# Optimization experiments

Measured on AMD Instinct MI355X. Metric: run time of the kernel, lower is better.

Reference implementation:

```python
import jax, jax.numpy as jnp
import numpy as np

N_NODES = 50000
N_EDGES = 1_600_000
N_GRAPHS = 64
EMB = 1280
GCN_DIMS = [128, 256, 256]
FC_DIMS = [1024, 128]
EPS = 1e-5  # BatchNorm eps (torch default)


def setup_inputs() -> dict:
    key = jax.random.key(0)
    ks = jax.random.split(key, 16)
    inp = {}
    inp["x"] = jax.random.normal(ks[0], (N_NODES, EMB), jnp.float32)
    inp["edge_index"] = jax.random.randint(ks[1], (2, N_EDGES), 0, N_NODES)
    inp["batch"] = jnp.sort(jax.random.randint(ks[2], (N_NODES,), 0, N_GRAPHS))
    dims = [EMB] + GCN_DIMS
    for i in range(3):
        inp[f"Wg{i}"] = jax.random.normal(ks[3 + i], (dims[i], dims[i + 1]), jnp.float32) * (1.0 / np.sqrt(dims[i]))
        inp[f"bg{i}"] = jnp.zeros((dims[i + 1],), jnp.float32)
        inp[f"gamma{i}"] = jnp.ones((dims[i + 1],), jnp.float32)
        inp[f"beta{i}"] = jnp.zeros((dims[i + 1],), jnp.float32)
    fdims = [GCN_DIMS[-1]] + FC_DIMS
    for i in range(2):
        inp[f"Wf{i}"] = jax.random.normal(ks[10 + i], (fdims[i], fdims[i + 1]), jnp.float32) * (1.0 / np.sqrt(fdims[i]))
        inp[f"bf{i}"] = jnp.zeros((fdims[i + 1],), jnp.float32)
    return inp


def _batchnorm(h, gamma, beta):
    # training-mode BN over node dim, biased variance (torch normalization)
    m = h.mean(axis=0)
    v = h.var(axis=0)
    return gamma * (h - m) * jax.lax.rsqrt(v + EPS) + beta


def reference(x, edge_index, batch,
              Wg0, bg0, gamma0, beta0,
              Wg1, bg1, gamma1, beta1,
              Wg2, bg2, gamma2, beta2,
              Wf0, bf0, Wf1, bf1):
    # --- GCN symmetric normalization with self-loops (PyG GCNConv default) ---
    loop = jnp.arange(N_NODES)
    src = jnp.concatenate([edge_index[0], loop])  # message sources
    dst = jnp.concatenate([edge_index[1], loop])  # aggregation targets
    deg = jax.ops.segment_sum(jnp.ones(src.shape[0], jnp.float32), dst, num_segments=N_NODES)
    dinv = jnp.where(deg > 0, jax.lax.rsqrt(jnp.maximum(deg, 1.0)), 0.0)
    norm = dinv[src] * dinv[dst]  # [E + N]

    def gcn_conv(h, W, b):
        h = h @ W                               # [N, d_out] transform first (PyG order)
        msg = h[src] * norm[:, None]            # gather + scale
        return jax.ops.segment_sum(msg, dst, num_segments=N_NODES) + b

    h = x
    for W, b, g, bt in ((Wg0, bg0, gamma0, beta0),
                        (Wg1, bg1, gamma1, beta1),
                        (Wg2, bg2, gamma2, beta2)):
        h = gcn_conv(h, W, b)
        h = _batchnorm(h, g, bt)
        h = jax.nn.relu(h)
        # dropout is identity in eval mode

    # --- global mean pool over graphs ---
    counts = jax.ops.segment_sum(jnp.ones(N_NODES, jnp.float32), batch, num_segments=N_GRAPHS)
    sums = jax.ops.segment_sum(h, batch, num_segments=N_GRAPHS)
    g = sums / jnp.maximum(counts, 1.0)[:, None]  # [B, 256]

    # --- FC head ---
    g = jax.nn.relu(g @ Wf0 + bf0)
    out = g @ Wf1 + bf1                           # [B, 128]
    return out
```

## Files before the change

### kernel.cpp

```cpp
#include <hip/hip_runtime.h>
#include <hip/hip_bf16.h>

#define N_NODES 50000
#define N_EDGES 1600000
#define N_GRAPHS 64

typedef _Float16 f16;
typedef _Float16 f16x8 __attribute__((ext_vector_type(8)));
typedef _Float16 f16x4 __attribute__((ext_vector_type(4)));
typedef _Float16 f16x2 __attribute__((ext_vector_type(2)));
typedef float f32x4 __attribute__((ext_vector_type(4)));

template <int V> struct VecT;
template <> struct VecT<2> { using type = f16x2; };
template <> struct VecT<4> { using type = f16x4; };

typedef __attribute__((address_space(3))) void lds_void_t;
typedef const __attribute__((address_space(1))) void gbl_void_t;
__device__ __forceinline__ void gload_lds16(const void* g, void* l) {
    __builtin_amdgcn_global_load_lds((gbl_void_t*)g, (lds_void_t*)l, 16, 0, 0);
}

__global__ void init_deg(int* deg) {
    int i = blockIdx.x * blockDim.x + threadIdx.x;
    if (i < N_NODES) deg[i] = 1;
}

__global__ void deg_count(const int* __restrict__ dst, int* __restrict__ deg) {
    int e = blockIdx.x * blockDim.x + threadIdx.x;
    if (e < N_EDGES) atomicAdd(&deg[dst[e]], 1);
}

__global__ void make_dinv(const int* __restrict__ deg, float* __restrict__ dinv) {
    int i = blockIdx.x * blockDim.x + threadIdx.x;
    if (i < N_NODES) dinv[i] = rsqrtf((float)deg[i]);
}

__global__ void scan_deg(const int* __restrict__ deg, int* __restrict__ rowstart,
                         int* __restrict__ pos) {
    __shared__ int wsum[16];
    __shared__ int carry_s;
    const int t = threadIdx.x;
    const int lane = t & 63;
    const int w = t >> 6;
    if (t == 0) carry_s = 0;
    __syncthreads();
    for (int base = 0; base < N_NODES; base += 1024) {
        int i = base + t;
        int v = (i < N_NODES) ? (deg[i] - 1) : 0;
        int s = v;
#pragma unroll
        for (int off = 1; off < 64; off <<= 1) {
            int n = __shfl_up(s, off, 64);
            if (lane >= off) s += n;
        }
        if (lane == 63) wsum[w] = s;
        __syncthreads();
        if (w == 0) {
            int ws = (lane < 16) ? wsum[lane] : 0;
#pragma unroll
            for (int off = 1; off < 16; off <<= 1) {
                int n = __shfl_up(ws, off, 64);
                if (lane >= off) ws += n;
            }
            if (lane < 16) wsum[lane] = ws;
        }
        __syncthreads();
        int waveoff = (w == 0) ? 0 : wsum[w - 1];
        int carry = carry_s;
        int excl = carry + waveoff + s - v;
        if (i < N_NODES) {
            rowstart[i] = excl;
            pos[i] = excl;
        }
        __syncthreads();
        if (t == 0) carry_s = carry + wsum[15];
        __syncthreads();
    }
    if (t == 0) rowstart[N_NODES] = carry_s;
}

__global__ void csr_fill(const int* __restrict__ src, const int* __restrict__ dst,
                         const float* __restrict__ dinv, int* __restrict__ pos,
                         int2* __restrict__ csr) {
    int e = blockIdx.x * blockDim.x + threadIdx.x;
    if (e >= N_EDGES) return;
    int s = src[e], d = dst[e];
    int slot = atomicAdd(&pos[d], 1);
    csr[slot] = make_int2(s, __float_as_int(dinv[s] * dinv[d]));
}

__global__ void cast_w(const float* __restrict__ W, f16* __restrict__ Wt, int K, int N) {
    int i = blockIdx.x * blockDim.x + threadIdx.x;
    if (i >= K * N) return;
    int k = i % K, n = i / K;
    Wt[i] = (f16)W[(size_t)k * N + n];
}

__launch_bounds__(256)
__global__ void gemm_x_lds(const float* __restrict__ A, const f16* __restrict__ Bt,
                           float* __restrict__ C0, float* __restrict__ C1, int M) {
    const int K = 1280;
    __shared__ float Asm[128 * 32];
    const int t = threadIdx.x;
    const int w = t >> 6, lane = t & 63;
    const int tile = blockIdx.x >> 1, s = blockIdx.x & 1;
    const int m0 = tile * 128;
    const int kbeg = s * 640;
    float* __restrict__ C = s ? C1 : C0;
    const int r = lane & 15, q = lane >> 4;

    const int rl_base = w * 32 + (lane >> 3);
    const int gchunk = (lane & 7) ^ ((lane >> 3) & 7);

    const int row_l0 = w * 32 + r;
    const int row_l1 = w * 32 + 16 + r;
    const int sw = r & 7;
    const float* lr0a = Asm + row_l0 * 32 + (((2 * q) ^ sw) << 2);
    const float* lr0b = Asm + row_l0 * 32 + (((2 * q + 1) ^ sw) << 2);
    const float* lr1a = Asm + row_l1 * 32 + (((2 * q) ^ sw) << 2);
    const float* lr1b = Asm + row_l1 * 32 + (((2 * q + 1) ^ sw) << 2);

    const f16* bp = Bt + (size_t)r * K + kbeg + q * 8;

    f32x4 acc[2][8];
#pragma unroll
    for (int i = 0; i < 2; ++i)
#pragma unroll
        for (int j = 0; j < 8; ++j) acc[i][j] = (f32x4){0.f, 0.f, 0.f, 0.f};

    for (int kt = 0; kt < 20; ++kt) {
        const int kk = kbeg + kt * 32;
#pragma unroll
        for (int i = 0; i < 4; ++i) {
            int row_g = m0 + rl_base + i * 8;
            row_g = row_g < M ? row_g : M - 1;
            const float* src = A + (size_t)row_g * K + kk + gchunk * 4;
            float* dst = Asm + (w * 32 + i * 8) * 32;
            gload_lds16(src, dst);
        }
        __syncthreads();
        float4 u0 = *(const float4*)lr0a;
        float4 v0 = *(const float4*)lr0b;
        float4 u1 = *(const float4*)lr1a;
        float4 v1 = *(const float4*)lr1b;
        f16x8 af0 = {(f16)u0.x, (f16)u0.y, (f16)u0.z, (f16)u0.w,
                     (f16)v0.x, (f16)v0.y, (f16)v0.z, (f16)v0.w};
        f16x8 af1 = {(f16)u1.x, (f16)u1.y, (f16)u1.z, (f16)u1.w,
                     (f16)v1.x, (f16)v1.y, (f16)v1.z, (f16)v1.w};
#pragma unroll
        for (int ni = 0; ni < 8; ++ni) {
            f16x8 bf = *(const f16x8*)(bp + (size_t)ni * 16 * K + kt * 32);
            acc[0][ni] = __builtin_amdgcn_mfma_f32_16x16x32_f16(af0, bf, acc[0][ni], 0, 0, 0);
            acc[1][ni] = __builtin_amdgcn_mfma_f32_16x16x32_f16(af1, bf, acc[1][ni], 0, 0, 0);
        }
        __syncthreads();
    }
#pragma unroll
    for (int mi = 0; mi < 2; ++mi)
#pragma unroll
        for (int j = 0; j < 4; ++j) {
            int row = m0 + w * 32 + mi * 16 + q * 4 + j;
            if (row < M) {
                float* cp = C + (size_t)row * 128 + r;
#pragma unroll
                for (int ni = 0; ni < 8; ++ni) cp[ni * 16] = acc[mi][ni][j];
            }
        }
}

__global__ void reduce_cast(const float* __restrict__ c0, const float* __restrict__ c1,
                            f16* __restrict__ o, int n4) {
    int i = blockIdx.x * blockDim.x + threadIdx.x;
    if (i >= n4) return;
    float4 a = ((const float4*)c0)[i];
    float4 b = ((const float4*)c1)[i];
    f16x4 r = {(f16)(a.x + b.x), (f16)(a.y + b.y), (f16)(a.z + b.z), (f16)(a.w + b.w)};
    ((f16x4*)o)[i] = r;
}

template <int K>
__launch_bounds__(256)
__global__ void gemm_h_bn_pipe(const f16* __restrict__ A16, const float* __restrict__ ss,
                               const f16* __restrict__ Bt, f16* __restrict__ C16, int N) {
    constexpr int NT = K / 32;
    const int gw = (int)((blockIdx.x * blockDim.x + threadIdx.x) >> 6);
    const int lane = threadIdx.x & 63;
    const int m0 = gw * 32;
    if (m0 >= N_NODES) return;
    const int col0 = blockIdx.y * 128;
    const int r = lane & 15, q = lane >> 4;
    int row0 = m0 + r;       row0 = row0 < N_NODES ? row0 : N_NODES - 1;
    int row1 = m0 + 16 + r;  row1 = row1 < N_NODES ? row1 : N_NODES - 1;
    const f16* a0 = A16 + (size_t)row0 * K + q * 8;
    const f16* a1 = A16 + (size_t)row1 * K + q * 8;
    const f16* bp = Bt + (size_t)(col0 + r) * K + q * 8;
    const float* scp = ss + q * 8;
    const float* shp = ss + K + q * 8;

    f32x4 acc[2][8];
#pragma unroll
    for (int i = 0; i < 2; ++i)
#pragma unroll
        for (int j = 0; j < 8; ++j) acc[i][j] = (f32x4){0.f, 0.f, 0.f, 0.f};

    f16x8 ab[2][2];
    f16x8 bb[2][8];
    float4 sb[2][4];
    ab[0][0] = *(const f16x8*)(a0);
    ab[0][1] = *(const f16x8*)(a1);
    sb[0][0] = *(const float4*)(scp);
    sb[0][1] = *(const float4*)(scp + 4);
    sb[0][2] = *(const float4*)(shp);
    sb[0][3] = *(const float4*)(shp + 4);
#pragma unroll
    for (int ni = 0; ni < 8; ++ni) bb[0][ni] = *(const f16x8*)(bp + (size_t)ni * 16 * K);

#pragma unroll
    for (int kt = 0; kt < NT; ++kt) {
        const int cur = kt & 1, nxt = cur ^ 1;
        if (kt < NT - 1) {
            const int ko = (kt + 1) * 32;
            ab[nxt][0] = *(const f16x8*)(a0 + ko);
            ab[nxt][1] = *(const f16x8*)(a1 + ko);
            sb[nxt][0] = *(const float4*)(scp + ko);
            sb[nxt][1] = *(const float4*)(scp + ko + 4);
            sb[nxt][2] = *(const float4*)(shp + ko);
            sb[nxt][3] = *(const float4*)(shp + ko + 4);
#pragma unroll
            for (int ni = 0; ni < 8; ++ni)
                bb[nxt][ni] = *(const f16x8*)(bp + (size_t)ni * 16 * K + ko);
        }
        float sc[8] = {sb[cur][0].x, sb[cur][0].y, sb[cur][0].z, sb[cur][0].w,
                       sb[cur][1].x, sb[cur][1].y, sb[cur][1].z, sb[cur][1].w};
        float sh[8] = {sb[cur][2].x, sb[cur][2].y, sb[cur][2].z, sb[cur][2].w,
                       sb[cur][3].x, sb[cur][3].y, sb[cur][3].z, sb[cur][3].w};
        f16x8 af0, af1;
#pragma unroll
        for (int j = 0; j < 8; ++j) {
            float v0 = (float)ab[cur][0][j] * sc[j] + sh[j];
            float v1 = (float)ab[cur][1][j] * sc[j] + sh[j];
            af0[j] = (f16)(v0 > 0.f ? v0 : 0.f);
            af1[j] = (f16)(v1 > 0.f ? v1 : 0.f);
        }
#pragma unroll
        for (int ni = 0; ni < 8; ++ni) {
            acc[0][ni] = __builtin_amdgcn_mfma_f32_16x16x32_f16(af0, bb[cur][ni], acc[0][ni], 0, 0, 0);
            acc[1][ni] = __builtin_amdgcn_mfma_f32_16x16x32_f16(af1, bb[cur][ni], acc[1][ni], 0, 0, 0);
        }
    }
#pragma unroll
    for (int mi = 0; mi < 2; ++mi)
#pragma unroll
        for (int j = 0; j < 4; ++j) {
            int row = m0 + mi * 16 + q * 4 + j;
            if (row < N_NODES) {
                f16* cp = C16 + (size_t)row * N + col0 + r;
#pragma unroll
                for (int ni = 0; ni < 8; ++ni) cp[ni * 16] = (f16)acc[mi][ni][j];
            }
        }
}

template <int D>
__launch_bounds__(256)
__global__ void aggregate(const f16* __restrict__ h, const int* __restrict__ rowstart,
                          const int2* __restrict__ csr, const float* __restrict__ dinv,
                          const float* __restrict__ bias, f16* __restrict__ out) {
    constexpr int V = D / 64;
    using vec = typename VecT<V>::type;
    int w = (int)((blockIdx.x * blockDim.x + threadIdx.x) >> 6);
    int lane = threadIdx.x & 63;
    if (w >= N_NODES) return;
    float acc[V];
    float di = dinv[w];
    vec self = *(const vec*)(h + (size_t)w * D + lane * V);
#pragma unroll
    for (int v = 0; v < V; ++v) acc[v] = (float)self[v] * (di * di);
    int e0 = rowstart[w], e1 = rowstart[w + 1];
    int j = e0;
    for (; j + 8 <= e1; j += 8) {
        int2 c[8];
        vec rr[8];
#pragma unroll
        for (int u = 0; u < 8; ++u) c[u] = csr[j + u];
#pragma unroll
        for (int u = 0; u < 8; ++u)
            rr[u] = *(const vec*)(h + (size_t)c[u].x * D + lane * V);
#pragma unroll
        for (int u = 0; u < 8; ++u) {
            float nm = __int_as_float(c[u].y);
#pragma unroll
            for (int v = 0; v < V; ++v) acc[v] += (float)rr[u][v] * nm;
        }
    }
    if (j + 4 <= e1) {
        int2 c0 = csr[j], c1 = csr[j + 1], c2 = csr[j + 2], c3 = csr[j + 3];
        vec r0 = *(const vec*)(h + (size_t)c0.x * D + lane * V);
        vec r1 = *(const vec*)(h + (size_t)c1.x * D + lane * V);
        vec r2 = *(const vec*)(h + (size_t)c2.x * D + lane * V);
        vec r3 = *(const vec*)(h + (size_t)c3.x * D + lane * V);
        float n0 = __int_as_float(c0.y), n1 = __int_as_float(c1.y);
        float n2 = __int_as_float(c2.y), n3 = __int_as_float(c3.y);
#pragma unroll
        for (int v = 0; v < V; ++v)
            acc[v] += (float)r0[v] * n0 + (float)r1[v] * n1 +
                      (float)r2[v] * n2 + (float)r3[v] * n3;
        j += 4;
    }
    for (; j < e1; ++j) {
        int2 c = csr[j];
        vec r = *(const vec*)(h + (size_t)c.x * D + lane * V);
        float nm = __int_as_float(c.y);
#pragma unroll
        for (int v = 0; v < V; ++v) acc[v] += (float)r[v] * nm;
    }
    vec o;
#pragma unroll
    for (int v = 0; v < V; ++v) o[v] = (f16)(acc[v] + bias[lane * V + v]);
    *(vec*)(out + (size_t)w * D + lane * V) = o;
}

template <int D>
__global__ void bn_stats(const f16* __restrict__ h, float* __restrict__ stat) {
    int f = threadIdx.x;
    int r0 = blockIdx.x * 128;
    int r1 = min(r0 + 128, N_NODES);
    float s = 0.f, s2 = 0.f;
    for (int r = r0; r < r1; ++r) {
        float v = (float)h[(size_t)r * D + f];
        s += v;
        s2 += v * v;
    }
    atomicAdd(&stat[f], s);
    atomicAdd(&stat[D + f], s2);
}

template <int D>
__global__ void bn_finalize(const float* __restrict__ stat, const float* __restrict__ gamma,
                            const float* __restrict__ beta, float* __restrict__ ss) {
    int f = threadIdx.x;
    float m = stat[f] * (1.0f / N_NODES);
    float var = stat[D + f] * (1.0f / N_NODES) - m * m;
    float sc = gamma[f] * rsqrtf(var + 1e-5f);
    ss[f] = sc;
    ss[D + f] = beta[f] - m * sc;
}

__global__ void count_batch_bs(const int* __restrict__ batch, int* __restrict__ cnt) {
    int g = threadIdx.x;
    if (g >= N_GRAPHS) return;
    int lo = 0, hi = N_NODES;
    while (lo < hi) { int mid = (lo + hi) >> 1; if (batch[mid] < g) lo = mid + 1; else hi = mid; }
    int b0 = lo;
    lo = 0; hi = N_NODES;
    while (lo < hi) { int mid = (lo + hi) >> 1; if (batch[mid] < g + 1) lo = mid + 1; else hi = mid; }
    cnt[g] = lo - b0;
}

__global__ void pool_seg_bn(const f16* __restrict__ h, const float* __restrict__ ss,
                            const int* __restrict__ batch, float* __restrict__ psum) {
    int f = threadIdx.x;
    float sc = ss[f], sh = ss[256 + f];
    int r0 = blockIdx.x * 64;
    int r1 = min(r0 + 64, N_NODES);
    float acc = 0.f;
    int cur = batch[r0];
    for (int r = r0; r < r1; ++r) {
        int b = batch[r];
        if (b != cur) {
            atomicAdd(&psum[cur * 256 + f], acc);
            acc = 0.f;
            cur = b;
        }
        float v = sc * (float)h[(size_t)r * 256 + f] + sh;
        acc += v > 0.f ? v : 0.f;
    }
    atomicAdd(&psum[cur * 256 + f], acc);
}

__global__ void pool_div(const float* __restrict__ psum, const int* __restrict__ cnt,
                         float* __restrict__ g) {
    int i = blockIdx.x * 256 + threadIdx.x;
    int b = i >> 8;
    float c = (float)max(cnt[b], 1);
    g[i] = psum[i] / c;
}

__global__ void fc_init(const float* __restrict__ b, float* __restrict__ Y, int rows, int N) {
    int i = blockIdx.x * blockDim.x + threadIdx.x;
    if (i < rows * N) Y[i] = b[i % N];
}

__global__ void fc_splitk(const float* __restrict__ X, const float* __restrict__ W,
                          float* __restrict__ Y, int K, int N, int KC) {
    int col = blockIdx.x * blockDim.x + threadIdx.x;
    int row = blockIdx.y;
    int k0 = blockIdx.z * KC;
    float acc = 0.f;
    const float* x = X + (size_t)row * K + k0;
    const float* w = W + (size_t)k0 * N + col;
#pragma unroll 8
    for (int k = 0; k < KC; ++k) acc += x[k] * w[(size_t)k * N];
    atomicAdd(&Y[(size_t)row * N + col], acc);
}

__global__ void relu_inplace(float* __restrict__ Y, int n) {
    int i = blockIdx.x * blockDim.x + threadIdx.x;
    if (i < n) Y[i] = Y[i] > 0.f ? Y[i] : 0.f;
}

extern "C" void kernel_launch(void* const* d_in, const int* in_sizes, int n_in,
                              void* d_out, int out_size, void* d_ws, size_t ws_size,
                              hipStream_t stream) {
    const float* x     = (const float*)d_in[0];
    const int*   ei    = (const int*)d_in[1];
    const int*   batch = (const int*)d_in[2];
    const float* Wg0 = (const float*)d_in[3],  *bg0 = (const float*)d_in[4];
    const float* gamma0 = (const float*)d_in[5], *beta0 = (const float*)d_in[6];
    const float* Wg1 = (const float*)d_in[7],  *bg1 = (const float*)d_in[8];
    const float* gamma1 = (const float*)d_in[9], *beta1 = (const float*)d_in[10];
    const float* Wg2 = (const float*)d_in[11], *bg2 = (const float*)d_in[12];
    const float* gamma2 = (const float*)d_in[13], *beta2 = (const float*)d_in[14];
    const float* Wf0 = (const float*)d_in[15], *bf0 = (const float*)d_in[16];
    const float* Wf1 = (const float*)d_in[17], *bf1 = (const float*)d_in[18];
    float* out = (float*)d_out;

    size_t off = 0;
    auto alloc = [&](size_t bytes) {
        void* p = (char*)d_ws + off;
        off += (bytes + 255) & ~(size_t)255;
        return p;
    };
    f16*   hA16     = (f16*)alloc((size_t)N_NODES * 256 * 2);
    float* cp32     = (float*)alloc((size_t)2 * N_NODES * 128 * 4);
    f16*   hBn16    = (f16*)cp32;
    float* cp0      = cp32;
    float* cp1      = cp32 + (size_t)N_NODES * 128;
    int2*  csr      = (int2*)alloc((size_t)N_EDGES * 8);
    int*   deg      = (int*)alloc((size_t)N_NODES * 4);
    float* dinv     = (float*)alloc((size_t)N_NODES * 4);
    int*   rowstart = (int*)alloc((size_t)(N_NODES + 1) * 4);
    int*   pos      = (int*)alloc((size_t)N_NODES * 4);
    float* bnstat   = (float*)alloc(2 * 256 * 4);
    float* bnss     = (float*)alloc(2 * 256 * 4);
    float* psum     = (float*)alloc(64 * 256 * 4);
    int*   pcount   = (int*)alloc(64 * 4);
    float* gpool    = (float*)alloc(64 * 256 * 4);
    float* g1       = (float*)alloc(64 * 1024 * 4);
    f16*   W0t      = (f16*)alloc((size_t)1280 * 128 * 2);
    f16*   W1t      = (f16*)alloc((size_t)128 * 256 * 2);
    f16*   W2t      = (f16*)alloc((size_t)256 * 256 * 2);
    (void)ws_size;

    const int TPB = 256;
    const int nb_nodes = (N_NODES + TPB - 1) / TPB;
    const int nb_edges = (N_EDGES + TPB - 1) / TPB;

    init_deg<<<nb_nodes, TPB, 0, stream>>>(deg);
    deg_count<<<nb_edges, TPB, 0, stream>>>(ei + N_EDGES, deg);
    make_dinv<<<nb_nodes, TPB, 0, stream>>>(deg, dinv);
    scan_deg<<<1, 1024, 0, stream>>>(deg, rowstart, pos);
    csr_fill<<<nb_edges, TPB, 0, stream>>>(ei, ei + N_EDGES, dinv, pos, csr);
    cast_w<<<(1280 * 128 + 255) / 256, 256, 0, stream>>>(Wg0, W0t, 1280, 128);
    cast_w<<<(128 * 256 + 255) / 256, 256, 0, stream>>>(Wg1, W1t, 128, 256);
    cast_w<<<(256 * 256 + 255) / 256, 256, 0, stream>>>(Wg2, W2t, 256, 256);

    const int tiles128 = (N_NODES + 127) / 128;
    const int gemm0_blocks = tiles128 * 2;
    const int gemmh_blocks = (1563 * 64 + TPB - 1) / TPB;
    const int agg_blocks = (N_NODES * 64 + TPB - 1) / TPB;

    gemm_x_lds<<<gemm0_blocks, TPB, 0, stream>>>(x, W0t, cp0, cp1, N_NODES);
    reduce_cast<<<(N_NODES * 128 / 4 + 255) / 256, 256, 0, stream>>>(cp0, cp1, hA16, N_NODES * 128 / 4);
    aggregate<128><<<agg_blocks, TPB, 0, stream>>>(hA16, rowstart, csr, dinv, bg0, hBn16);
    hipMemsetAsync(bnstat, 0, 2 * 128 * 4, stream);
    bn_stats<128><<<(N_NODES + 127) / 128, 128, 0, stream>>>(hBn16, bnstat);
    bn_finalize<128><<<1, 128, 0, stream>>>(bnstat, gamma0, beta0, bnss);

    gemm_h_bn_pipe<128><<<dim3(gemmh_blocks, 2), TPB, 0, stream>>>(hBn16, bnss, W1t, hA16, 256);
    aggregate<256><<<agg_blocks, TPB, 0, stream>>>(hA16, rowstart, csr, dinv, bg1, hBn16);
    hipMemsetAsync(bnstat, 0, 2 * 256 * 4, stream);
    bn_stats<256><<<(N_NODES + 127) / 128, 256, 0, stream>>>(hBn16, bnstat);
    bn_finalize<256><<<1, 256, 0, stream>>>(bnstat, gamma1, beta1, bnss);

    gemm_h_bn_pipe<256><<<dim3(gemmh_blocks, 2), TPB, 0, stream>>>(hBn16, bnss, W2t, hA16, 256);
    aggregate<256><<<agg_blocks, TPB, 0, stream>>>(hA16, rowstart, csr, dinv, bg2, hBn16);
    hipMemsetAsync(bnstat, 0, 2 * 256 * 4, stream);
    bn_stats<256><<<(N_NODES + 127) / 128, 256, 0, stream>>>(hBn16, bnstat);
    bn_finalize<256><<<1, 256, 0, stream>>>(bnstat, gamma2, beta2, bnss);

    hipMemsetAsync(psum, 0, 64 * 256 * 4, stream);
    count_batch_bs<<<1, 64, 0, stream>>>(batch, pcount);
    pool_seg_bn<<<(N_NODES + 63) / 64, 256, 0, stream>>>(hBn16, bnss, batch, psum);
    pool_div<<<64, 256, 0, stream>>>(psum, pcount, gpool);

    fc_init<<<(64 * 1024 + 255) / 256, 256, 0, stream>>>(bf0, g1, 64, 1024);
    fc_splitk<<<dim3(4, 64, 4), 256, 0, stream>>>(gpool, Wf0, g1, 256, 1024, 64);
    relu_inplace<<<(64 * 1024 + 255) / 256, 256, 0, stream>>>(g1, 64 * 1024);
    fc_init<<<(64 * 128 + 255) / 256, 256, 0, stream>>>(bf1, out, 64, 128);
    fc_splitk<<<dim3(1, 64, 16), 128, 0, stream>>>(g1, Wf1, out, 1024, 128, 64);
}
```

Measured before the change: 857.9 us.

## Double-buffer per-wave LDS staging in X GEMM and drop block barriers

The first-layer GEMM now gives each wave its own pair of LDS buffers. It prefetches the next K-tile with global_load_lds while computing on the current one and waits with vmcnt counters instead of block-wide __syncthreads. Because each wave only reads rows it staged itself, the barriers are removed. This is meant to hide global load latency and remove sync stalls. It doubles LDS use, and it relies on vmcnt ordering, with the B-operand global loads also counted, to guarantee the LDS data is ready, which is fragile.

```diff
diff --git a/kernel.cpp b/kernel.cpp
--- a/kernel.cpp
+++ b/kernel.cpp
@@ -101,7 +101,7 @@
 __global__ void gemm_x_lds(const float* __restrict__ A, const f16* __restrict__ Bt,
                            float* __restrict__ C0, float* __restrict__ C1, int M) {
     const int K = 1280;
-    __shared__ float Asm[128 * 32];
+    __shared__ float Asm[4][2][32 * 32];
     const int t = threadIdx.x;
     const int w = t >> 6, lane = t & 63;
     const int tile = blockIdx.x >> 1, s = blockIdx.x & 1;
@@ -110,16 +110,14 @@
     float* __restrict__ C = s ? C1 : C0;
     const int r = lane & 15, q = lane >> 4;
 
-    const int rl_base = w * 32 + (lane >> 3);
-    const int gchunk = (lane & 7) ^ ((lane >> 3) & 7);
-
-    const int row_l0 = w * 32 + r;
-    const int row_l1 = w * 32 + 16 + r;
+    const int rl = lane >> 3;
+    const int gchunk = (lane & 7) ^ (rl & 7);
+
     const int sw = r & 7;
-    const float* lr0a = Asm + row_l0 * 32 + (((2 * q) ^ sw) << 2);
-    const float* lr0b = Asm + row_l0 * 32 + (((2 * q + 1) ^ sw) << 2);
-    const float* lr1a = Asm + row_l1 * 32 + (((2 * q) ^ sw) << 2);
-    const float* lr1b = Asm + row_l1 * 32 + (((2 * q + 1) ^ sw) << 2);
+    const int off0a = r * 32 + (((2 * q) ^ sw) << 2);
+    const int off0b = r * 32 + (((2 * q + 1) ^ sw) << 2);
+    const int off1a = (16 + r) * 32 + (((2 * q) ^ sw) << 2);
+    const int off1b = (16 + r) * 32 + (((2 * q + 1) ^ sw) << 2);
 
     const f16* bp = Bt + (size_t)r * K + kbeg + q * 8;
 
@@ -129,21 +127,35 @@
 #pragma unroll
         for (int j = 0; j < 8; ++j) acc[i][j] = (f32x4){0.f, 0.f, 0.f, 0.f};
 
+    float* buf0 = &Asm[w][0][0];
+    float* buf1 = &Asm[w][1][0];
+
+    auto STAGE = [&](float* buf, int kt) {
+        const int kk = kbeg + kt * 32;
+#pragma unroll
+        for (int i = 0; i < 4; ++i) {
+            int row_g = m0 + w * 32 + i * 8 + rl;
+            row_g = row_g < M ? row_g : M - 1;
+            gload_lds16(A + (size_t)row_g * K + kk + gchunk * 4, buf + i * 256);
+        }
+    };
+
+    STAGE(buf0, 0);
+#pragma unroll 2
     for (int kt = 0; kt < 20; ++kt) {
-        const int kk = kbeg + kt * 32;
-#pragma unroll
-        for (int i = 0; i < 4; ++i) {
-            int row_g = m0 + rl_base + i * 8;
-            row_g = row_g < M ? row_g : M - 1;
-            const float* src = A + (size_t)row_g * K + kk + gchunk * 4;
-            float* dst = Asm + (w * 32 + i * 8) * 32;
-            gload_lds16(src, dst);
-        }
-        __syncthreads();
-        float4 u0 = *(const float4*)lr0a;
-        float4 v0 = *(const float4*)lr0b;
-        float4 u1 = *(const float4*)lr1a;
-        float4 v1 = *(const float4*)lr1b;
+        float* cur = (kt & 1) ? buf1 : buf0;
+        float* nxt = (kt & 1) ? buf0 : buf1;
+        if (kt < 19) {
+            STAGE(nxt, kt + 1);
+            asm volatile("s_waitcnt vmcnt(4)" ::: "memory");
+        } else {
+            asm volatile("s_waitcnt vmcnt(0)" ::: "memory");
+        }
+        __builtin_amdgcn_sched_barrier(0);
+        float4 u0 = *(const float4*)(cur + off0a);
+        float4 v0 = *(const float4*)(cur + off0b);
+        float4 u1 = *(const float4*)(cur + off1a);
+        float4 v1 = *(const float4*)(cur + off1b);
         f16x8 af0 = {(f16)u0.x, (f16)u0.y, (f16)u0.z, (f16)u0.w,
                      (f16)v0.x, (f16)v0.y, (f16)v0.z, (f16)v0.w};
         f16x8 af1 = {(f16)u1.x, (f16)u1.y, (f16)u1.z, (f16)u1.w,
@@ -154,7 +166,6 @@
             acc[0][ni] = __builtin_amdgcn_mfma_f32_16x16x32_f16(af0, bf, acc[0][ni], 0, 0, 0);
             acc[1][ni] = __builtin_amdgcn_mfma_f32_16x16x32_f16(af1, bf, acc[1][ni], 0, 0, 0);
         }
-        __syncthreads();
     }
 #pragma unroll
     for (int mi = 0; mi < 2; ++mi)
```

After: 870.0 us, median of 2. About the same (+1.4%).

## Split GCN aggregation into 32-feature column slices for cache locality

Applied to the files above, without the earlier changes.

Replaces the single full-width aggregation kernel with multiple launches, each gathering a 32-column slice of the feature matrix per node. The intent is to shrink each pass's random-gather working set so it stays in L2. In exchange the CSR and row offsets are re-read once per slice, and half of each wavefront's lanes sit idle. Gathers also become narrower, so edge-traversal work is multiplied by the slice count.

```diff
diff --git a/kernel.cpp b/kernel.cpp
--- a/kernel.cpp
+++ b/kernel.cpp
@@ -10,10 +10,6 @@
 typedef _Float16 f16x4 __attribute__((ext_vector_type(4)));
 typedef _Float16 f16x2 __attribute__((ext_vector_type(2)));
 typedef float f32x4 __attribute__((ext_vector_type(4)));
-
-template <int V> struct VecT;
-template <> struct VecT<2> { using type = f16x2; };
-template <> struct VecT<4> { using type = f16x4; };
 
 typedef __attribute__((address_space(3))) void lds_void_t;
 typedef const __attribute__((address_space(1))) void gbl_void_t;
@@ -264,61 +260,33 @@
 
 template <int D>
 __launch_bounds__(256)
-__global__ void aggregate(const f16* __restrict__ h, const int* __restrict__ rowstart,
-                          const int2* __restrict__ csr, const float* __restrict__ dinv,
-                          const float* __restrict__ bias, f16* __restrict__ out) {
-    constexpr int V = D / 64;
-    using vec = typename VecT<V>::type;
+__global__ void aggregate_slice(const f16* __restrict__ h, const int* __restrict__ rowstart,
+                                const int2* __restrict__ csr, const float* __restrict__ dinv,
+                                const float* __restrict__ bias, f16* __restrict__ out,
+                                int p32) {
     int w = (int)((blockIdx.x * blockDim.x + threadIdx.x) >> 6);
     int lane = threadIdx.x & 63;
-    if (w >= N_NODES) return;
-    float acc[V];
+    if (w >= N_NODES || lane >= 32) return;
+    const f16* hs = h + p32 + lane;
     float di = dinv[w];
-    vec self = *(const vec*)(h + (size_t)w * D + lane * V);
-#pragma unroll
-    for (int v = 0; v < V; ++v) acc[v] = (float)self[v] * (di * di);
+    float acc = (float)hs[(size_t)w * D] * (di * di);
     int e0 = rowstart[w], e1 = rowstart[w + 1];
     int j = e0;
     for (; j + 8 <= e1; j += 8) {
         int2 c[8];
-        vec rr[8];
+        float rv[8];
 #pragma unroll
         for (int u = 0; u < 8; ++u) c[u] = csr[j + u];
 #pragma unroll
-        for (int u = 0; u < 8; ++u)
-            rr[u] = *(const vec*)(h + (size_t)c[u].x * D + lane * V);
-#pragma unroll
-        for (int u = 0; u < 8; ++u) {
-            float nm = __int_as_float(c[u].y);
-#pragma unroll
-            for (int v = 0; v < V; ++v) acc[v] += (float)rr[u][v] * nm;
-        }
-    }
-    if (j + 4 <= e1) {
-        int2 c0 = csr[j], c1 = csr[j + 1], c2 = csr[j + 2], c3 = csr[j + 3];
-        vec r0 = *(const vec*)(h + (size_t)c0.x * D + lane * V);
-        vec r1 = *(const vec*)(h + (size_t)c1.x * D + lane * V);
-        vec r2 = *(const vec*)(h + (size_t)c2.x * D + lane * V);
-        vec r3 = *(const vec*)(h + (size_t)c3.x * D + lane * V);
-        float n0 = __int_as_float(c0.y), n1 = __int_as_float(c1.y);
-        float n2 = __int_as_float(c2.y), n3 = __int_as_float(c3.y);
-#pragma unroll
-        for (int v = 0; v < V; ++v)
-            acc[v] += (float)r0[v] * n0 + (float)r1[v] * n1 +
-                      (float)r2[v] * n2 + (float)r3[v] * n3;
-        j += 4;
+        for (int u = 0; u < 8; ++u) rv[u] = (float)hs[(size_t)c[u].x * D];
+#pragma unroll
+        for (int u = 0; u < 8; ++u) acc += rv[u] * __int_as_float(c[u].y);
     }
     for (; j < e1; ++j) {
         int2 c = csr[j];
-        vec r = *(const vec*)(h + (size_t)c.x * D + lane * V);
-        float nm = __int_as_float(c.y);
-#pragma unroll
-        for (int v = 0; v < V; ++v) acc[v] += (float)r[v] * nm;
-    }
-    vec o;
-#pragma unroll
-    for (int v = 0; v < V; ++v) o[v] = (f16)(acc[v] + bias[lane * V + v]);
-    *(vec*)(out + (size_t)w * D + lane * V) = o;
+        acc += (float)hs[(size_t)c.x * D] * __int_as_float(c.y);
+    }
+    out[(size_t)w * D + p32 + lane] = (f16)(acc + bias[p32 + lane]);
 }
 
 template <int D>
@@ -469,23 +437,26 @@
     const int tiles128 = (N_NODES + 127) / 128;
     const int gemm0_blocks = tiles128 * 2;
     const int gemmh_blocks = (1563 * 64 + TPB - 1) / TPB;
-    const int agg_blocks = (N_NODES * 64 + TPB - 1) / TPB;
+    const int agg_blocks = (N_NODES + 3) / 4;
 
     gemm_x_lds<<<gemm0_blocks, TPB, 0, stream>>>(x, W0t, cp0, cp1, N_NODES);
     reduce_cast<<<(N_NODES * 128 / 4 + 255) / 256, 256, 0, stream>>>(cp0, cp1, hA16, N_NODES * 128 / 4);
-    aggregate<128><<<agg_blocks, TPB, 0, stream>>>(hA16, rowstart, csr, dinv, bg0, hBn16);
+    for (int p = 0; p < 4; ++p)
+        aggregate_slice<128><<<agg_blocks, TPB, 0, stream>>>(hA16, rowstart, csr, dinv, bg0, hBn16, p * 32);
     hipMemsetAsync(bnstat, 0, 2 * 128 * 4, stream);
     bn_stats<128><<<(N_NODES + 127) / 128, 128, 0, stream>>>(hBn16, bnstat);
     bn_finalize<128><<<1, 128, 0, stream>>>(bnstat, gamma0, beta0, bnss);
 
     gemm_h_bn_pipe<128><<<dim3(gemmh_blocks, 2), TPB, 0, stream>>>(hBn16, bnss, W1t, hA16, 256);
-    aggregate<256><<<agg_blocks, TPB, 0, stream>>>(hA16, rowstart, csr, dinv, bg1, hBn16);
+    for (int p = 0; p < 8; ++p)
+        aggregate_slice<256><<<agg_blocks, TPB, 0, stream>>>(hA16, rowstart, csr, dinv, bg1, hBn16, p * 32);
     hipMemsetAsync(bnstat, 0, 2 * 256 * 4, stream);
     bn_stats<256><<<(N_NODES + 127) / 128, 256, 0, stream>>>(hBn16, bnstat);
     bn_finalize<256><<<1, 256, 0, stream>>>(bnstat, gamma1, beta1, bnss);
 
     gemm_h_bn_pipe<256><<<dim3(gemmh_blocks, 2), TPB, 0, stream>>>(hBn16, bnss, W2t, hA16, 256);
-    aggregate<256><<<agg_blocks, TPB, 0, stream>>>(hA16, rowstart, csr, dinv, bg2, hBn16);
+    for (int p = 0; p < 8; ++p)
+        aggregate_slice<256><<<agg_blocks, TPB, 0, stream>>>(hA16, rowstart, csr, dinv, bg2, hBn16, p * 32);
     hipMemsetAsync(bnstat, 0, 2 * 256 * 4, stream);
     bn_stats<256><<<(N_NODES + 127) / 128, 256, 0, stream>>>(hBn16, bnstat);
     bn_finalize<256><<<1, 256, 0, stream>>>(bnstat, gamma2, beta2, bnss);
```

Measured after the change: 1.594 ms. +85.8%, slower.

## Reorder layer-1 GCN to aggregate before transform on narrower features

Applied to the files above, without the earlier changes.

For the second GCN layer, BN+ReLU is applied as a separate elementwise pass, the sparse aggregation runs on the 128-wide input features, and only afterwards is the 128→256 GEMM applied with the bias added in its epilogue. This exploits linearity of aggregation to halve the bytes gathered per edge in that layer. In exchange it adds an extra elementwise kernel and a full read/write of the normalized activations, and it changes the fp16 rounding order.

```diff
diff --git a/kernel.cpp b/kernel.cpp
--- a/kernel.cpp
+++ b/kernel.cpp
@@ -262,7 +262,70 @@
         }
 }
 
-template <int D>
+template <int K>
+__launch_bounds__(256)
+__global__ void gemm_h_bias_pipe(const f16* __restrict__ A16, const f16* __restrict__ Bt,
+                                 const float* __restrict__ bias, f16* __restrict__ C16, int N) {
+    constexpr int NT = K / 32;
+    const int gw = (int)((blockIdx.x * blockDim.x + threadIdx.x) >> 6);
+    const int lane = threadIdx.x & 63;
+    const int m0 = gw * 32;
+    if (m0 >= N_NODES) return;
+    const int col0 = blockIdx.y * 128;
+    const int r = lane & 15, q = lane >> 4;
+    int row0 = m0 + r;       row0 = row0 < N_NODES ? row0 : N_NODES - 1;
+    int row1 = m0 + 16 + r;  row1 = row1 < N_NODES ? row1 : N_NODES - 1;
+    const f16* a0 = A16 + (size_t)row0 * K + q * 8;
+    const f16* a1 = A16 + (size_t)row1 * K + q * 8;
+    const f16* bp = Bt + (size_t)(col0 + r) * K + q * 8;
+
+    f32x4 acc[2][8];
+#pragma unroll
+    for (int i = 0; i < 2; ++i)
+#pragma unroll
+        for (int j = 0; j < 8; ++j) acc[i][j] = (f32x4){0.f, 0.f, 0.f, 0.f};
+
+    f16x8 ab[2][2];
+    f16x8 bb[2][8];
+    ab[0][0] = *(const f16x8*)(a0);
+    ab[0][1] = *(const f16x8*)(a1);
+#pragma unroll
+    for (int ni = 0; ni < 8; ++ni) bb[0][ni] = *(const f16x8*)(bp + (size_t)ni * 16 * K);
+
+#pragma unroll
+    for (int kt = 0; kt < NT; ++kt) {
+        const int cur = kt & 1, nxt = cur ^ 1;
+        if (kt < NT - 1) {
+            const int ko = (kt + 1) * 32;
+            ab[nxt][0] = *(const f16x8*)(a0 + ko);
+            ab[nxt][1] = *(const f16x8*)(a1 + ko);
+#pragma unroll
+            for (int ni = 0; ni < 8; ++ni)
+                bb[nxt][ni] = *(const f16x8*)(bp + (size_t)ni * 16 * K + ko);
+        }
+#pragma unroll
+        for (int ni = 0; ni < 8; ++ni) {
+            acc[0][ni] = __builtin_amdgcn_mfma_f32_16x16x32_f16(ab[cur][0], bb[cur][ni], acc[0][ni], 0, 0, 0);
+            acc[1][ni] = __builtin_amdgcn_mfma_f32_16x16x32_f16(ab[cur][1], bb[cur][ni], acc[1][ni], 0, 0, 0);
+        }
+    }
+    float bv[8];
+#pragma unroll
+    for (int ni = 0; ni < 8; ++ni) bv[ni] = bias[col0 + ni * 16 + r];
+#pragma unroll
+    for (int mi = 0; mi < 2; ++mi)
+#pragma unroll
+        for (int j = 0; j < 4; ++j) {
+            int row = m0 + mi * 16 + q * 4 + j;
+            if (row < N_NODES) {
+                f16* cp = C16 + (size_t)row * N + col0 + r;
+#pragma unroll
+                for (int ni = 0; ni < 8; ++ni) cp[ni * 16] = (f16)(acc[mi][ni][j] + bv[ni]);
+            }
+        }
+}
+
+template <int D, bool BIAS>
 __launch_bounds__(256)
 __global__ void aggregate(const f16* __restrict__ h, const int* __restrict__ rowstart,
                           const int2* __restrict__ csr, const float* __restrict__ dinv,
@@ -317,7 +380,8 @@
     }
     vec o;
 #pragma unroll
-    for (int v = 0; v < V; ++v) o[v] = (f16)(acc[v] + bias[lane * V + v]);
+    for (int v = 0; v < V; ++v)
+        o[v] = (f16)(BIAS ? (acc[v] + bias[lane * V + v]) : acc[v]);
     *(vec*)(out + (size_t)w * D + lane * V) = o;
 }
 
@@ -345,6 +409,22 @@
     float sc = gamma[f] * rsqrtf(var + 1e-5f);
     ss[f] = sc;
     ss[D + f] = beta[f] - m * sc;
+}
+
+template <int D>
+__global__ void bn_apply_relu(const f16* __restrict__ hin, const float* __restrict__ ss,
+                              f16* __restrict__ hout) {
+    int i = blockIdx.x * blockDim.x + threadIdx.x;
+    if (i >= N_NODES * D / 8) return;
+    int f0 = (i * 8) & (D - 1);
+    f16x8 v = ((const f16x8*)hin)[i];
+    f16x8 r;
+#pragma unroll
+    for (int j = 0; j < 8; ++j) {
+        float val = (float)v[j] * ss[f0 + j] + ss[D + f0 + j];
+        r[j] = (f16)(val > 0.f ? val : 0.f);
+    }
+    ((f16x8*)hout)[i] = r;
 }
 
 __global__ void count_batch_bs(const int* __restrict__ batch, int* __restrict__ cnt) {
@@ -437,6 +517,8 @@
     f16*   hBn16    = (f16*)cp32;
     float* cp0      = cp32;
     float* cp1      = cp32 + (size_t)N_NODES * 128;
+    f16*   h16      = hA16;
+    f16*   agg16    = hA16 + (size_t)N_NODES * 128;
     int2*  csr      = (int2*)alloc((size_t)N_EDGES * 8);
     int*   deg      = (int*)alloc((size_t)N_NODES * 4);
     float* dinv     = (float*)alloc((size_t)N_NODES * 4);
@@ -473,19 +555,20 @@
 
     gemm_x_lds<<<gemm0_blocks, TPB, 0, stream>>>(x, W0t, cp0, cp1, N_NODES);
     reduce_cast<<<(N_NODES * 128 / 4 + 255) / 256, 256, 0, stream>>>(cp0, cp1, hA16, N_NODES * 128 / 4);
-    aggregate<128><<<agg_blocks, TPB, 0, stream>>>(hA16, rowstart, csr, dinv, bg0, hBn16);
+    aggregate<128, true><<<agg_blocks, TPB, 0, stream>>>(hA16, rowstart, csr, dinv, bg0, hBn16);
     hipMemsetAsync(bnstat, 0, 2 * 128 * 4, stream);
     bn_stats<128><<<(N_NODES + 127) / 128, 128, 0, stream>>>(hBn16, bnstat);
     bn_finalize<128><<<1, 128, 0, stream>>>(bnstat, gamma0, beta0, bnss);
 
-    gemm_h_bn_pipe<128><<<dim3(gemmh_blocks, 2), TPB, 0, stream>>>(hBn16, bnss, W1t, hA16, 256);
-    aggregate<256><<<agg_blocks, TPB, 0, stream>>>(hA16, rowstart, csr, dinv, bg1, hBn16);
+    bn_apply_relu<128><<<(N_NODES * 128 / 8 + 255) / 256, 256, 0, stream>>>(hBn16, bnss, h16);
+    aggregate<128, false><<<agg_blocks, TPB, 0, stream>>>(h16, rowstart, csr, dinv, nullptr, agg16);
+    gemm_h_bias_pipe<128><<<dim3(gemmh_blocks, 2), TPB, 0, stream>>>(agg16, W1t, bg1, hBn16, 256);
     hipMemsetAsync(bnstat, 0, 2 * 256 * 4, stream);
     bn_stats<256><<<(N_NODES + 127) / 128, 256, 0, stream>>>(hBn16, bnstat);
     bn_finalize<256><<<1, 256, 0, stream>>>(bnstat, gamma1, beta1, bnss);
 
     gemm_h_bn_pipe<256><<<dim3(gemmh_blocks, 2), TPB, 0, stream>>>(hBn16, bnss, W2t, hA16, 256);
-    aggregate<256><<<agg_blocks, TPB, 0, stream>>>(hA16, rowstart, csr, dinv, bg2, hBn16);
+    aggregate<256, true><<<agg_blocks, TPB, 0, stream>>>(hA16, rowstart, csr, dinv, bg2, hBn16);
     hipMemsetAsync(bnstat, 0, 2 * 256 * 4, stream);
     bn_stats<256><<<(N_NODES + 127) / 128, 256, 0, stream>>>(hBn16, bnstat);
     bn_finalize<256><<<1, 256, 0, stream>>>(bnstat, gamma2, beta2, bnss);
```

New measurement: 811.2 us. -5.4%, faster.
